# Kernel optimization log

Hardware: AMD Instinct MI355X
Metric: run time of the kernel (lower is better)

The kernel has to match this reference:

```python
import jax, jax.numpy as jnp
import numpy as np

N = 100000       # nodes
E = 3200000      # directed edges (before self-loops)
F_IN = 256       # num_node_features
HID = 8          # hidden per head (conv1)
HEADS = 8        # conv1 heads
C_OUT = 1        # conv2 out channels / heads=1


def setup_inputs() -> dict:
    key = jax.random.key(0)
    ks = jax.random.split(key, 10)
    s = 0.1
    return {
        "x": jax.random.normal(ks[0], (N, F_IN), jnp.float32),
        "edge_index": jax.random.randint(ks[1], (2, E), 0, N, dtype=jnp.int32),
        "W1": jax.random.normal(ks[2], (F_IN, HEADS * HID), jnp.float32) * s,
        "att_src1": jax.random.normal(ks[3], (HEADS, HID), jnp.float32) * s,
        "att_dst1": jax.random.normal(ks[4], (HEADS, HID), jnp.float32) * s,
        "b1": jnp.zeros((HEADS * HID,), jnp.float32),
        "W2": jax.random.normal(ks[5], (HEADS * HID, C_OUT), jnp.float32) * s,
        "att_src2": jax.random.normal(ks[6], (1, C_OUT), jnp.float32) * s,
        "att_dst2": jax.random.normal(ks[7], (1, C_OUT), jnp.float32) * s,
        "b2": jnp.zeros((C_OUT,), jnp.float32),
    }


def gat_conv(x, W, att_src, att_dst, bias, src, dst, heads, out_ch, concat):
    # PyG GATConv (eval mode): h = x @ W per head; alpha over incoming edges of dst.
    h = (x @ W).reshape(-1, heads, out_ch)                 # [N, H, C]
    a_s = jnp.einsum('nhc,hc->nh', h, att_src)             # source term
    a_d = jnp.einsum('nhc,hc->nh', h, att_dst)             # target term
    e = jax.nn.leaky_relu(a_s[src] + a_d[dst], 0.2)        # [Etot, H]
    # segment softmax over edges grouped by target node
    m = jax.ops.segment_max(e, dst, num_segments=N)
    ex = jnp.exp(e - m[dst])
    denom = jax.ops.segment_sum(ex, dst, num_segments=N)
    alpha = ex / (denom[dst] + 1e-16)                      # [Etot, H]
    out = jax.ops.segment_sum(h[src] * alpha[..., None], dst, num_segments=N)
    out = out.reshape(-1, heads * out_ch) if concat else out.mean(axis=1)
    return out + bias


def reference(x, edge_index, W1, att_src1, att_dst1, b1, W2, att_src2, att_dst2, b2):
    # add self-loops (GATConv default add_self_loops=True)
    loop = jnp.arange(N, dtype=edge_index.dtype)
    src = jnp.concatenate([edge_index[0], loop])
    dst = jnp.concatenate([edge_index[1], loop])
    # dropout layers are identity in eval mode
    h = gat_conv(x, W1, att_src1, att_dst1, b1, src, dst, HEADS, HID, True)
    h = jax.nn.elu(h)
    out = gat_conv(h, W2, att_src2, att_dst2, b2, src, dst, 1, C_OUT, False)
    return jax.nn.sigmoid(out)
```

## Files before the change

kernel.cpp:

```cpp
#include <hip/hip_runtime.h>
#include <math.h>

#define FIN 256
#define C1  64
#define NH  8
#define HID 8
#define MAXBUK 512
#define CAPLOG 14
#define SC_CHUNK 8192
#define EPT (SC_CHUNK / 512)
#define NSLICE 8
#define SLDIV 12500u

typedef unsigned short ushort_t;
typedef unsigned int uint_t;
typedef __attribute__((ext_vector_type(8))) short short8;
typedef __attribute__((ext_vector_type(4))) float f32x4;

__device__ __forceinline__ ushort_t f2bf(float f) {
    uint_t u = __float_as_uint(f);
    u += 0x7fffu + ((u >> 16) & 1u);
    return (ushort_t)(u >> 16);
}
__device__ __forceinline__ uint_t packbf2(float lo, float hi) {
    return (uint_t)f2bf(lo) | ((uint_t)f2bf(hi) << 16);
}
__device__ __forceinline__ float bf_lo(uint_t w) { return __uint_as_float(w << 16); }
__device__ __forceinline__ float bf_hi(uint_t w) { return __uint_as_float(w & 0xffff0000u); }

__global__ void k_prep(const float* __restrict__ W, ushort_t* __restrict__ Wtg,
                       int* __restrict__ bkt_cnt) {
    int tid = blockIdx.x * 256 + threadIdx.x;
    if (tid < MAXBUK) bkt_cnt[tid] = 0;
    int c = tid >> 8;
    int k = tid & 255;
    Wtg[c * 256 + k] = f2bf(W[k * C1 + c]);
}

__global__ __launch_bounds__(512) void k_bscatter(const int* __restrict__ ei, int E, int N,
                                                  int NBUK, int* __restrict__ bkt_cnt,
                                                  uint_t* __restrict__ ebuf) {
    __shared__ int hist[MAXBUK];
    __shared__ int loff[MAXBUK];
    __shared__ int delta[MAXBUK];
    __shared__ int ssum[MAXBUK];
    __shared__ uint_t vals[SC_CHUNK];
    __shared__ ushort_t buks[SC_CHUNK];

    const int t = threadIdx.x;
    hist[t] = 0;
    __syncthreads();

    const int Etot = E + N;
    const int base0 = blockIdx.x * SC_CHUNK;
    const int lim = min(base0 + SC_CHUNK, Etot);
    const int cnt = lim - base0;

    uint_t myval[EPT];
    int myb[EPT];
#pragma unroll
    for (int i = 0; i < EPT; ++i) {
        int e = base0 + t + i * 512;
        if (e < lim) {
            int s, d;
            if (e < E) { s = ei[e]; d = ei[E + e]; } else { s = e - E; d = s; }
            myval[i] = ((uint_t)s << 8) | (uint_t)(d & 255);
            myb[i] = d >> 8;
            atomicAdd(&hist[myb[i]], 1);
        } else myb[i] = -1;
    }
    __syncthreads();

    int v = hist[t];
    ssum[t] = v;
    __syncthreads();
    for (int o = 1; o < 512; o <<= 1) {
        int add = (t >= o) ? ssum[t - o] : 0;
        __syncthreads();
        ssum[t] += add;
        __syncthreads();
    }
    loff[t] = ssum[t] - v;
    __syncthreads();

    if (t < NBUK) {
        int c = hist[t];
        if (c) delta[t] = (t << CAPLOG) + atomicAdd(&bkt_cnt[t], c) - loff[t];
    }
    __syncthreads();

#pragma unroll
    for (int i = 0; i < EPT; ++i) {
        if (myb[i] >= 0) {
            int pos = atomicAdd(&loff[myb[i]], 1);
            vals[pos] = myval[i];
            buks[pos] = (ushort_t)myb[i];
        }
    }
    __syncthreads();

    for (int i = t; i < cnt; i += 512)
        ebuf[delta[buks[i]] + i] = vals[i];
}

__global__ __launch_bounds__(512) void k_bucket_csr(const uint_t* __restrict__ ebuf,
                                                    const int* __restrict__ bkt_cnt, int N,
                                                    int* __restrict__ deg, int* __restrict__ off,
                                                    int* __restrict__ csr) {
    __shared__ int hist[256 * NSLICE];
    __shared__ int ssum[512];
    int b = blockIdx.x;
    int t = threadIdx.x;
    int beg = b << CAPLOG;
    int end = beg + bkt_cnt[b];
    for (int i = t; i < 256 * NSLICE; i += 512) hist[i] = 0;
    __syncthreads();
    for (int j = beg + t; j < end; j += 512) {
        uint_t v = ebuf[j];
        int key = ((v & 255u) << 3) | ((v >> 8) / SLDIV);
        atomicAdd(&hist[key], 1);
    }
    __syncthreads();
    if (t < 256) {
        int node = (b << 8) + t;
        if (node < N) {
            int s = 0;
#pragma unroll
            for (int i = 0; i < 8; ++i) s += hist[(t << 3) | i];
            deg[node] = s;
        }
    }
    int c0 = hist[4 * t], c1 = hist[4 * t + 1], c2 = hist[4 * t + 2], c3 = hist[4 * t + 3];
    int s4 = c0 + c1 + c2 + c3;
    __syncthreads();
    ssum[t] = s4;
    __syncthreads();
    for (int o = 1; o < 512; o <<= 1) {
        int add = (t >= o) ? ssum[t - o] : 0;
        __syncthreads();
        ssum[t] += add;
        __syncthreads();
    }
    int base = beg + ssum[t] - s4;
    hist[4 * t]     = base;
    hist[4 * t + 1] = base + c0;
    hist[4 * t + 2] = base + c0 + c1;
    hist[4 * t + 3] = base + c0 + c1 + c2;
    __syncthreads();
    if (t < 256) {
        int node = (b << 8) + t;
        if (node < N) off[node] = hist[t << 3];
    }
    __syncthreads();
    for (int j = beg + t; j < end; j += 512) {
        uint_t v = ebuf[j];
        int key = ((v & 255u) << 3) | ((v >> 8) / SLDIV);
        int pos = atomicAdd(&hist[key], 1);
        csr[pos] = (int)(v >> 8);
    }
}

__global__ __launch_bounds__(256) void k_gemm1(
    const float* __restrict__ x, const ushort_t* __restrict__ Wtg,
    const float* __restrict__ att_s, const float* __restrict__ att_d,
    ushort_t* __restrict__ h1b, ushort_t* __restrict__ as1b, float* __restrict__ ad1, int N)
{
    const int t = threadIdx.x;
    const int wv = t >> 6, l = t & 63;
    const int l15 = l & 15, q = l >> 4;
    const int node = blockIdx.x * 64 + wv * 16 + l15;
    const bool ok = node < N;
    const float* xr = x + (size_t)(ok ? node : N - 1) * FIN;

    f32x4 acc[4];
#pragma unroll
    for (int ct = 0; ct < 4; ++ct) acc[ct] = (f32x4){0.f, 0.f, 0.f, 0.f};

    for (int kk = 0; kk < 8; ++kk) {
        const int kof = kk * 32 + q * 8;
        short8 af[4];
#pragma unroll
        for (int ct = 0; ct < 4; ++ct)
            af[ct] = *reinterpret_cast<const short8*>(&Wtg[(ct * 16 + l15) * 256 + kof]);
        const float4* xp = reinterpret_cast<const float4*>(xr + kof);
        float4 v0 = xp[0], v1 = xp[1];
        union { short8 s; uint_t u[4]; } bu;
        bu.u[0] = packbf2(v0.x, v0.y);
        bu.u[1] = packbf2(v0.z, v0.w);
        bu.u[2] = packbf2(v1.x, v1.y);
        bu.u[3] = packbf2(v1.z, v1.w);
#pragma unroll
        for (int ct = 0; ct < 4; ++ct)
            acc[ct] = __builtin_amdgcn_mfma_f32_16x16x32_bf16(af[ct], bu.s, acc[ct], 0, 0, 0);
    }

    float4 ats[4], atd4[4];
#pragma unroll
    for (int ct = 0; ct < 4; ++ct) {
        ats[ct]  = *reinterpret_cast<const float4*>(&att_s[ct * 16 + q * 4]);
        atd4[ct] = *reinterpret_cast<const float4*>(&att_d[ct * 16 + q * 4]);
    }
    const int hb = q >> 1;

    float asp[8], adp[8];
#pragma unroll
    for (int h = 0; h < 8; ++h) { asp[h] = 0.f; adp[h] = 0.f; }
#pragma unroll
    for (int ct = 0; ct < 4; ++ct) {
        f32x4 a = acc[ct];
        if (ok) {
            uint2 hv;
            hv.x = packbf2(a[0], a[1]);
            hv.y = packbf2(a[2], a[3]);
            *reinterpret_cast<uint2*>(&h1b[(size_t)node * C1 + ct * 16 + q * 4]) = hv;
        }
        int h = ct * 2 + hb;
        asp[h] = a[0] * ats[ct].x + a[1] * ats[ct].y + a[2] * ats[ct].z + a[3] * ats[ct].w;
        adp[h] = a[0] * atd4[ct].x + a[1] * atd4[ct].y + a[2] * atd4[ct].z + a[3] * atd4[ct].w;
    }
#pragma unroll
    for (int o = 16; o <= 32; o <<= 1) {
#pragma unroll
        for (int h = 0; h < 8; ++h) {
            asp[h] += __shfl_xor(asp[h], o, 64);
            adp[h] += __shfl_xor(adp[h], o, 64);
        }
    }
    if (q == 0 && ok) {
        uint4 aw;
        aw.x = packbf2(asp[0], asp[1]);
        aw.y = packbf2(asp[2], asp[3]);
        aw.z = packbf2(asp[4], asp[5]);
        aw.w = packbf2(asp[6], asp[7]);
        *reinterpret_cast<uint4*>(&as1b[(size_t)node * NH]) = aw;
        *reinterpret_cast<float4*>(&ad1[(size_t)node * NH]) =
            make_float4(adp[0], adp[1], adp[2], adp[3]);
        *reinterpret_cast<float4*>(&ad1[(size_t)node * NH + 4]) =
            make_float4(adp[4], adp[5], adp[6], adp[7]);
    }
}

__global__ __launch_bounds__(256) void k_agg1(
    const int* __restrict__ csr, const int* __restrict__ off, const int* __restrict__ deg,
    const ushort_t* __restrict__ as1b, const float* __restrict__ ad1,
    const ushort_t* __restrict__ h1b,
    const float* __restrict__ b1, const float* __restrict__ W2,
    float* __restrict__ h2, int N)
{
    int idx = blockIdx.x * 256 + threadIdx.x;
    int n = idx >> 4;
    if (n >= N) return;
    int sub  = threadIdx.x & 15;
    int hp   = sub & 3;
    int slot = sub >> 2;

    int beg = off[n];
    int end = beg + deg[n];

    float adv0 = ad1[(size_t)n * NH + 2 * hp];
    float adv1 = ad1[(size_t)n * NH + 2 * hp + 1];
    float den0 = 0.f, den1 = 0.f;
    float acc[16];
#pragma unroll
    for (int k = 0; k < 16; ++k) acc[k] = 0.f;

    for (int base = beg; base < end; base += 4) {
        int j = base + slot;
        int jj = j < end ? j : end - 1;
        int s = csr[jj];
        uint_t a2 = *reinterpret_cast<const uint_t*>(&as1b[(size_t)s * NH + 2 * hp]);
        float t0 = bf_lo(a2) + adv0;
        float t1 = bf_hi(a2) + adv1;
        t0 = fmaxf(t0, 0.2f * t0);
        t1 = fmaxf(t1, 0.2f * t1);
        bool live = j < end;
        float ex0 = live ? __expf(t0) : 0.f;
        float ex1 = live ? __expf(t1) : 0.f;
        den0 += ex0; den1 += ex1;
        const uint4* hbp = reinterpret_cast<const uint4*>(&h1b[(size_t)s * C1 + hp * 16]);
        uint4 u0 = hbp[0], u1 = hbp[1];
        acc[0]  = fmaf(ex0, bf_lo(u0.x), acc[0]);
        acc[1]  = fmaf(ex0, bf_hi(u0.x), acc[1]);
        acc[2]  = fmaf(ex0, bf_lo(u0.y), acc[2]);
        acc[3]  = fmaf(ex0, bf_hi(u0.y), acc[3]);
        acc[4]  = fmaf(ex0, bf_lo(u0.z), acc[4]);
        acc[5]  = fmaf(ex0, bf_hi(u0.z), acc[5]);
        acc[6]  = fmaf(ex0, bf_lo(u0.w), acc[6]);
        acc[7]  = fmaf(ex0, bf_hi(u0.w), acc[7]);
        acc[8]  = fmaf(ex1, bf_lo(u1.x), acc[8]);
        acc[9]  = fmaf(ex1, bf_hi(u1.x), acc[9]);
        acc[10] = fmaf(ex1, bf_lo(u1.y), acc[10]);
        acc[11] = fmaf(ex1, bf_hi(u1.y), acc[11]);
        acc[12] = fmaf(ex1, bf_lo(u1.z), acc[12]);
        acc[13] = fmaf(ex1, bf_hi(u1.z), acc[13]);
        acc[14] = fmaf(ex1, bf_lo(u1.w), acc[14]);
        acc[15] = fmaf(ex1, bf_hi(u1.w), acc[15]);
    }

#pragma unroll
    for (int o = 4; o <= 8; o <<= 1) {
        den0 += __shfl_xor(den0, o, 64);
        den1 += __shfl_xor(den1, o, 64);
#pragma unroll
        for (int k = 0; k < 16; ++k) acc[k] += __shfl_xor(acc[k], o, 64);
    }

    float inv0 = 1.f / (den0 + 1e-16f);
    float inv1 = 1.f / (den1 + 1e-16f);
    const float4* bp = reinterpret_cast<const float4*>(&b1[hp * 16]);
    const float4* wp = reinterpret_cast<const float4*>(&W2[hp * 16]);
    float bb[16], ww[16];
#pragma unroll
    for (int i = 0; i < 4; ++i) {
        float4 b4 = bp[i], w4 = wp[i];
        bb[4 * i] = b4.x; bb[4 * i + 1] = b4.y; bb[4 * i + 2] = b4.z; bb[4 * i + 3] = b4.w;
        ww[4 * i] = w4.x; ww[4 * i + 1] = w4.y; ww[4 * i + 2] = w4.z; ww[4 * i + 3] = w4.w;
    }
    float p = 0.f;
#pragma unroll
    for (int k = 0; k < 16; ++k) {
        float inv = (k < 8) ? inv0 : inv1;
        float v = acc[k] * inv + bb[k];
        v = v > 0.f ? v : (__expf(v) - 1.f);
        p = fmaf(v, ww[k], p);
    }
#pragma unroll
    for (int o = 1; o <= 2; o <<= 1) p += __shfl_xor(p, o, 64);
    if (sub == 0) h2[n] = p;
}

__global__ __launch_bounds__(256) void k_agg2(
    const int* __restrict__ csr, const int* __restrict__ off, const int* __restrict__ deg,
    const float* __restrict__ h2,
    const float* __restrict__ ats2, const float* __restrict__ atd2,
    const float* __restrict__ b2, float* __restrict__ out, int N)
{
    int idx = blockIdx.x * 256 + threadIdx.x;
    int n = idx >> 4;
    int l16 = threadIdx.x & 15;
    if (n >= N) return;
    int beg = off[n];
    int end = beg + deg[n];
    float a_s = ats2[0], a_d = atd2[0];
    float adv = h2[n] * a_d;
    float den = 0.f, num = 0.f;
    for (int j = beg + l16; j < end; j += 16) {
        float hs = h2[csr[j]];
        float t = fmaf(hs, a_s, adv);
        t = fmaxf(t, 0.2f * t);
        float ex = __expf(t);
        den += ex;
        num = fmaf(ex, hs, num);
    }
#pragma unroll
    for (int o = 1; o <= 8; o <<= 1) {
        den += __shfl_xor(den, o, 64);
        num += __shfl_xor(num, o, 64);
    }
    if (l16 == 0) {
        float t = num / (den + 1e-16f) + b2[0];
        out[n] = 1.f / (1.f + __expf(-t));
    }
}

extern "C" void kernel_launch(void* const* d_in, const int* in_sizes, int n_in,
                              void* d_out, int out_size, void* d_ws, size_t ws_size,
                              hipStream_t stream)
{
    const float* x    = (const float*)d_in[0];
    const int*   ei   = (const int*)d_in[1];
    const float* W1   = (const float*)d_in[2];
    const float* ats1 = (const float*)d_in[3];
    const float* atd1 = (const float*)d_in[4];
    const float* b1   = (const float*)d_in[5];
    const float* W2   = (const float*)d_in[6];
    const float* ats2 = (const float*)d_in[7];
    const float* atd2 = (const float*)d_in[8];
    const float* b2   = (const float*)d_in[9];
    float* out = (float*)d_out;

    const int N = out_size;
    const int E = in_sizes[1] / 2;
    const int Etot = E + N;
    const int NBUK = (N + 255) >> 8;
    const size_t capElems = (size_t)NBUK << CAPLOG;

    char* base = (char*)d_ws;
    uint_t* ebuf = (uint_t*)base;
    ushort_t* h1b  = (ushort_t*)base;
    ushort_t* as1b = h1b + (size_t)N * C1;
    float* ad1 = (float*)(as1b + (size_t)N * NH);
    float* h2  = ad1 + (size_t)N * NH;
    size_t featBytes = (size_t)N * (C1 * 2 + NH * 2 + NH * 4 + 4);
    size_t unionBytes = capElems * sizeof(uint_t);
    if (featBytes > unionBytes) unionBytes = featBytes;
    unionBytes = (unionBytes + 255) & ~(size_t)255;
    int* deg     = (int*)(base + unionBytes);
    int* off     = deg + N;
    int* bkt_cnt = off + N;
    int* csr     = bkt_cnt + MAXBUK;
    ushort_t* wtg = (ushort_t*)(csr + capElems);

    k_prep<<<64, 256, 0, stream>>>(W1, wtg, bkt_cnt);
    k_bscatter<<<(Etot + SC_CHUNK - 1) / SC_CHUNK, 512, 0, stream>>>(ei, E, N, NBUK, bkt_cnt, ebuf);
    k_bucket_csr<<<NBUK, 512, 0, stream>>>(ebuf, bkt_cnt, N, deg, off, csr);

    k_gemm1<<<(N + 63) / 64, 256, 0, stream>>>(x, wtg, ats1, atd1, h1b, as1b, ad1, N);
    k_agg1<<<(N * 16 + 255) / 256, 256, 0, stream>>>(csr, off, deg, as1b, ad1, h1b, b1, W2, h2, N);
    k_agg2<<<(N * 16 + 255) / 256, 256, 0, stream>>>(csr, off, deg, h2, ats2, atd2, b2, out, N);
}
```

Before: 330.3 us.

## Co-schedule GEMM1 blocks with edge bucketing kernels and use wave-shuffle scans

Merges the bucket-scatter and bucket-CSR kernels with halves of the layer-1 GEMM into two combined kernels. Block index picks the role, so the memory-bound graph build and the compute-heavy projection run concurrently instead of back to back. Separates the edge buffer from the feature buffers, since they now coexist and can no longer share memory. Replaces the LDS Hillis-Steele scans with a wave-shuffle plus per-wave-offset exclusive scan, cutting barriers. GEMM blocks now run at 512 threads covering 128 nodes and share the scatter's large LDS allocation, which may lower occupancy.

New measurement: 328.8 us. About the same (-0.4%).

```diff
diff --git a/kernel.cpp b/kernel.cpp
--- a/kernel.cpp
+++ b/kernel.cpp
@@ -28,6 +28,22 @@
 __device__ __forceinline__ float bf_lo(uint_t w) { return __uint_as_float(w << 16); }
 __device__ __forceinline__ float bf_hi(uint_t w) { return __uint_as_float(w & 0xffff0000u); }
 
+__device__ __forceinline__ int exscan512(int v, int* lds8, int t) {
+    int lane = t & 63, w = t >> 6;
+    int sc = v;
+#pragma unroll
+    for (int o = 1; o < 64; o <<= 1) {
+        int u = __shfl_up(sc, o, 64);
+        if (lane >= o) sc += u;
+    }
+    if (lane == 63) lds8[w] = sc;
+    __syncthreads();
+    int woff = 0;
+#pragma unroll
+    for (int i = 0; i < 8; ++i) woff += (i < w) ? lds8[i] : 0;
+    return woff + sc - v;
+}
+
 __global__ void k_prep(const float* __restrict__ W, ushort_t* __restrict__ Wtg,
                        int* __restrict__ bkt_cnt) {
     int tid = blockIdx.x * 256 + threadIdx.x;
@@ -37,22 +53,21 @@
     Wtg[c * 256 + k] = f2bf(W[k * C1 + c]);
 }
 
-__global__ __launch_bounds__(512) void k_bscatter(const int* __restrict__ ei, int E, int N,
-                                                  int NBUK, int* __restrict__ bkt_cnt,
-                                                  uint_t* __restrict__ ebuf) {
-    __shared__ int hist[MAXBUK];
-    __shared__ int loff[MAXBUK];
-    __shared__ int delta[MAXBUK];
-    __shared__ int ssum[MAXBUK];
-    __shared__ uint_t vals[SC_CHUNK];
-    __shared__ ushort_t buks[SC_CHUNK];
+__device__ void dev_bscatter(const int* __restrict__ ei, int E, int N, int NBUK,
+                             int* __restrict__ bkt_cnt, uint_t* __restrict__ ebuf,
+                             char* smem, int bid) {
+    int* hist = (int*)smem;
+    int* loff = (int*)(smem + 2048);
+    int* lds8 = (int*)(smem + 4096);
+    uint_t* vals = (uint_t*)(smem + 4160);
+    ushort_t* buks = (ushort_t*)(smem + 36928);
 
     const int t = threadIdx.x;
     hist[t] = 0;
     __syncthreads();
 
     const int Etot = E + N;
-    const int base0 = blockIdx.x * SC_CHUNK;
+    const int base0 = bid * SC_CHUNK;
     const int lim = min(base0 + SC_CHUNK, Etot);
     const int cnt = lim - base0;
 
@@ -72,20 +87,13 @@
     __syncthreads();
 
     int v = hist[t];
-    ssum[t] = v;
-    __syncthreads();
-    for (int o = 1; o < 512; o <<= 1) {
-        int add = (t >= o) ? ssum[t - o] : 0;
-        __syncthreads();
-        ssum[t] += add;
-        __syncthreads();
-    }
-    loff[t] = ssum[t] - v;
+    int ex = exscan512(v, lds8, t);
+    loff[t] = ex;
     __syncthreads();
 
     if (t < NBUK) {
         int c = hist[t];
-        if (c) delta[t] = (t << CAPLOG) + atomicAdd(&bkt_cnt[t], c) - loff[t];
+        if (c) hist[t] = (t << CAPLOG) + atomicAdd(&bkt_cnt[t], c) - ex;
     }
     __syncthreads();
 
@@ -100,16 +108,14 @@
     __syncthreads();
 
     for (int i = t; i < cnt; i += 512)
-        ebuf[delta[buks[i]] + i] = vals[i];
-}
-
-__global__ __launch_bounds__(512) void k_bucket_csr(const uint_t* __restrict__ ebuf,
-                                                    const int* __restrict__ bkt_cnt, int N,
-                                                    int* __restrict__ deg, int* __restrict__ off,
-                                                    int* __restrict__ csr) {
-    __shared__ int hist[256 * NSLICE];
-    __shared__ int ssum[512];
-    int b = blockIdx.x;
+        ebuf[hist[buks[i]] + i] = vals[i];
+}
+
+__device__ void dev_bucket_csr(const uint_t* __restrict__ ebuf, const int* __restrict__ bkt_cnt,
+                               int N, int* __restrict__ deg, int* __restrict__ off,
+                               int* __restrict__ csr, char* smem, int b) {
+    int* hist = (int*)smem;
+    int* lds8 = (int*)(smem + 8192);
     int t = threadIdx.x;
     int beg = b << CAPLOG;
     int end = beg + bkt_cnt[b];
@@ -126,22 +132,13 @@
         if (node < N) {
             int s = 0;
 #pragma unroll
-            for (int i = 0; i < 8; ++i) s += hist[(t << 3) | i];
+            for (int i = 0; i < NSLICE; ++i) s += hist[(t << 3) | i];
             deg[node] = s;
         }
     }
     int c0 = hist[4 * t], c1 = hist[4 * t + 1], c2 = hist[4 * t + 2], c3 = hist[4 * t + 3];
     int s4 = c0 + c1 + c2 + c3;
-    __syncthreads();
-    ssum[t] = s4;
-    __syncthreads();
-    for (int o = 1; o < 512; o <<= 1) {
-        int add = (t >= o) ? ssum[t - o] : 0;
-        __syncthreads();
-        ssum[t] += add;
-        __syncthreads();
-    }
-    int base = beg + ssum[t] - s4;
+    int base = beg + exscan512(s4, lds8, t);
     hist[4 * t]     = base;
     hist[4 * t + 1] = base + c0;
     hist[4 * t + 2] = base + c0 + c1;
@@ -160,15 +157,14 @@
     }
 }
 
-__global__ __launch_bounds__(256) void k_gemm1(
-    const float* __restrict__ x, const ushort_t* __restrict__ Wtg,
-    const float* __restrict__ att_s, const float* __restrict__ att_d,
-    ushort_t* __restrict__ h1b, ushort_t* __restrict__ as1b, float* __restrict__ ad1, int N)
-{
+__device__ void dev_gemm1(const float* __restrict__ x, const ushort_t* __restrict__ Wtg,
+                          const float* __restrict__ att_s, const float* __restrict__ att_d,
+                          ushort_t* __restrict__ h1b, ushort_t* __restrict__ as1b,
+                          float* __restrict__ ad1, int N, int nodeBase512) {
     const int t = threadIdx.x;
     const int wv = t >> 6, l = t & 63;
     const int l15 = l & 15, q = l >> 4;
-    const int node = blockIdx.x * 64 + wv * 16 + l15;
+    const int node = nodeBase512 + wv * 16 + l15;
     const bool ok = node < N;
     const float* xr = x + (size_t)(ok ? node : N - 1) * FIN;
 
@@ -238,6 +234,37 @@
         *reinterpret_cast<float4*>(&ad1[(size_t)node * NH + 4]) =
             make_float4(adp[4], adp[5], adp[6], adp[7]);
     }
+}
+
+__global__ __launch_bounds__(512) void k_fatA(
+    const int* __restrict__ ei, int E, int N, int NBUK, int* __restrict__ bkt_cnt,
+    uint_t* __restrict__ ebuf,
+    const float* __restrict__ x, const ushort_t* __restrict__ Wtg,
+    const float* __restrict__ ats, const float* __restrict__ atd,
+    ushort_t* __restrict__ h1b, ushort_t* __restrict__ as1b, float* __restrict__ ad1,
+    int nbsc)
+{
+    __shared__ __align__(16) char smem[53312];
+    if ((int)blockIdx.x < nbsc)
+        dev_bscatter(ei, E, N, NBUK, bkt_cnt, ebuf, smem, blockIdx.x);
+    else
+        dev_gemm1(x, Wtg, ats, atd, h1b, as1b, ad1, N, ((int)blockIdx.x - nbsc) * 128);
+}
+
+__global__ __launch_bounds__(512) void k_fatB(
+    const uint_t* __restrict__ ebuf, const int* __restrict__ bkt_cnt, int N,
+    int* __restrict__ deg, int* __restrict__ off, int* __restrict__ csr,
+    const float* __restrict__ x, const ushort_t* __restrict__ Wtg,
+    const float* __restrict__ ats, const float* __restrict__ atd,
+    ushort_t* __restrict__ h1b, ushort_t* __restrict__ as1b, float* __restrict__ ad1,
+    int nbuk, int nodeOfs)
+{
+    __shared__ __align__(16) char smem[8256];
+    if ((int)blockIdx.x < nbuk)
+        dev_bucket_csr(ebuf, bkt_cnt, N, deg, off, csr, smem, blockIdx.x);
+    else
+        dev_gemm1(x, Wtg, ats, atd, h1b, as1b, ad1, N,
+                  nodeOfs + ((int)blockIdx.x - nbuk) * 128);
 }
 
 __global__ __launch_bounds__(256) void k_agg1(
@@ -387,25 +414,30 @@
 
     char* base = (char*)d_ws;
     uint_t* ebuf = (uint_t*)base;
-    ushort_t* h1b  = (ushort_t*)base;
+    size_t ebufBytes = (capElems * sizeof(uint_t) + 255) & ~(size_t)255;
+    ushort_t* h1b  = (ushort_t*)(base + ebufBytes);
     ushort_t* as1b = h1b + (size_t)N * C1;
     float* ad1 = (float*)(as1b + (size_t)N * NH);
     float* h2  = ad1 + (size_t)N * NH;
-    size_t featBytes = (size_t)N * (C1 * 2 + NH * 2 + NH * 4 + 4);
-    size_t unionBytes = capElems * sizeof(uint_t);
-    if (featBytes > unionBytes) unionBytes = featBytes;
-    unionBytes = (unionBytes + 255) & ~(size_t)255;
-    int* deg     = (int*)(base + unionBytes);
+    char* pend = (char*)(h2 + N);
+    size_t featEnd = ((size_t)(pend - base) + 255) & ~(size_t)255;
+    int* deg     = (int*)(base + featEnd);
     int* off     = deg + N;
     int* bkt_cnt = off + N;
     int* csr     = bkt_cnt + MAXBUK;
     ushort_t* wtg = (ushort_t*)(csr + capElems);
 
+    const int nbsc = (Etot + SC_CHUNK - 1) / SC_CHUNK;
+    const int halfNodes = (((N / 2) + 127) / 128) * 128;
+    const int ga = halfNodes / 128;
+    const int gb = (N - halfNodes + 127) / 128;
+
     k_prep<<<64, 256, 0, stream>>>(W1, wtg, bkt_cnt);
-    k_bscatter<<<(Etot + SC_CHUNK - 1) / SC_CHUNK, 512, 0, stream>>>(ei, E, N, NBUK, bkt_cnt, ebuf);
-    k_bucket_csr<<<NBUK, 512, 0, stream>>>(ebuf, bkt_cnt, N, deg, off, csr);
-
-    k_gemm1<<<(N + 63) / 64, 256, 0, stream>>>(x, wtg, ats1, atd1, h1b, as1b, ad1, N);
+    k_fatA<<<nbsc + ga, 512, 0, stream>>>(ei, E, N, NBUK, bkt_cnt, ebuf,
+                                          x, wtg, ats1, atd1, h1b, as1b, ad1, nbsc);
+    k_fatB<<<NBUK + gb, 512, 0, stream>>>(ebuf, bkt_cnt, N, deg, off, csr,
+                                          x, wtg, ats1, atd1, h1b, as1b, ad1,
+                                          NBUK, halfNodes);
     k_agg1<<<(N * 16 + 255) / 256, 256, 0, stream>>>(csr, off, deg, as1b, ad1, h1b, b1, W2, h2, N);
     k_agg2<<<(N * 16 + 255) / 256, 256, 0, stream>>>(csr, off, deg, h2, ats2, atd2, b2, out, N);
 }
```
